# Kernel optimization log

Measured on AMD Instinct MI355X. Metric: run time of the kernel, lower is better.

Reference implementation:

```python
import jax, jax.numpy as jnp
import numpy as np

B, T, C = 4, 2048, 1024
E, F, K = 8, 2048, 2


def setup_inputs() -> dict:
    key = jax.random.key(0)
    k0, k1, k2, k3 = jax.random.split(key, 4)
    s = lambda d: 1.0 / np.sqrt(d)
    x = jax.random.normal(k0, (B, T, C), dtype=jnp.float32)
    Wr = jax.random.normal(k1, (E, C), dtype=jnp.float32) * s(C)      # router: nn.Linear(C, E) weight [E, C]
    W1 = jax.random.normal(k2, (E, 2 * F, C), dtype=jnp.float32) * s(C)  # per-expert w1 [2F, C]
    W2 = jax.random.normal(k3, (E, C, F), dtype=jnp.float32) * s(F)      # per-expert w2 [C, F]
    return {"x": x, "Wr": Wr, "W1": W1, "W2": W2}


def reference(x, Wr, W1, W2):
    Bb, Tt, Cc = x.shape
    flat = x.reshape(-1, Cc)                         # [N, C]
    N = flat.shape[0]
    # router: top-k then softmax over the k selected logits
    logits = flat @ Wr.T                             # [N, E]
    weights, ids = jax.lax.top_k(logits, K)          # [N, K]
    weights = jax.nn.softmax(weights, axis=-1)
    rows = jnp.arange(N)[:, None]
    router_weights = jnp.zeros((N, E), dtype=flat.dtype).at[rows, ids].add(weights)  # [N, E]
    # all experts on all tokens (dense reference), SwiGLU
    h = jnp.einsum('nc,efc->nef', flat, W1)          # [N, E, 2F]
    val, gate = h[..., :F], h[..., F:]
    act = val * jax.nn.silu(gate)                    # [N, E, F]
    expert_outputs = jnp.einsum('nef,ecf->nec', act, W2)  # [N, E, C]
    out = jnp.einsum('nec,ne->nc', expert_outputs, router_weights)
    return out.reshape(Bb, Tt, Cc)
```

## Files before the change

### kernel.cpp

```cpp
#include <hip/hip_runtime.h>

#define NTOK 8192
#define CDIM 1024
#define FDIM 2048
#define NEXP 8
#define CAP  16384
#define NPAIR 16384
#define MTCAP 32

typedef __bf16 bf16x8 __attribute__((ext_vector_type(8)));
typedef float  f32x4  __attribute__((ext_vector_type(4)));

__device__ __forceinline__ unsigned short f2bf(float f) {
    unsigned int u = __builtin_bit_cast(unsigned int, f);
    unsigned int r = (u + 0x7FFFu + ((u >> 16) & 1u)) >> 16;
    return (unsigned short)r;
}

__device__ __forceinline__ unsigned int pack2(float lo, float hi) {
    return ((unsigned int)f2bf(hi) << 16) | (unsigned int)f2bf(lo);
}

__device__ __forceinline__ float bflo(unsigned int u) {
    return __builtin_bit_cast(float, u << 16);
}
__device__ __forceinline__ float bfhi(unsigned int u) {
    return __builtin_bit_cast(float, u & 0xFFFF0000u);
}

__device__ __forceinline__ void gload_lds16(const void* g, void* l) {
    __builtin_amdgcn_global_load_lds(
        (const __attribute__((address_space(1))) unsigned int*)g,
        (__attribute__((address_space(3))) unsigned int*)l, 16, 0, 0);
}

#define BARRIER() asm volatile("s_barrier" ::: "memory")
#define WAIT_LGKM0() do { asm volatile("s_waitcnt lgkmcnt(0)" ::: "memory"); __builtin_amdgcn_sched_barrier(0); } while (0)
#define WAITVM0() asm volatile("s_waitcnt vmcnt(0)" ::: "memory")

__global__ void cvt_kernel(const float* __restrict__ s, unsigned short* __restrict__ d, long ngrp) {
    long i = (long)blockIdx.x * blockDim.x + threadIdx.x;
    long stride = (long)gridDim.x * blockDim.x;
    const float4* s4 = (const float4*)s;
    uint4* d4 = (uint4*)d;
    for (long g = i; g < ngrp; g += stride) {
        float4 a = s4[2 * g], b = s4[2 * g + 1];
        uint4 o;
        o.x = pack2(a.x, a.y); o.y = pack2(a.z, a.w);
        o.z = pack2(b.x, b.y); o.w = pack2(b.z, b.w);
        d4[g] = o;
    }
}

__global__ __launch_bounds__(256) void logits_kernel(
    const float* __restrict__ x, const float* __restrict__ Wr,
    float* __restrict__ wgt, int* __restrict__ eids)
{
    int w = threadIdx.x >> 6, l = threadIdx.x & 63;
    int t = blockIdx.x * 4 + w;
    const float* xr = x + (size_t)t * CDIM;
    float acc[NEXP];
    #pragma unroll
    for (int e = 0; e < NEXP; e++) acc[e] = 0.f;
    for (int c = l; c < CDIM; c += 64) {
        float xv = xr[c];
        #pragma unroll
        for (int e = 0; e < NEXP; e++) acc[e] += xv * Wr[e * CDIM + c];
    }
    #pragma unroll
    for (int e = 0; e < NEXP; e++)
        for (int off = 32; off > 0; off >>= 1) acc[e] += __shfl_down(acc[e], off);
    if (l == 0) {
        int i0 = 0; float l0 = acc[0];
        #pragma unroll
        for (int e = 1; e < NEXP; e++) if (acc[e] > l0) { l0 = acc[e]; i0 = e; }
        int i1 = -1; float l1 = -3.4e38f;
        #pragma unroll
        for (int e = 0; e < NEXP; e++) if (e != i0 && acc[e] > l1) { l1 = acc[e]; i1 = e; }
        float tv = __expf(l1 - l0);
        float den = 1.f + tv;
        wgt[2 * t] = 1.f / den;
        wgt[2 * t + 1] = tv / den;
        eids[t] = i0 | (i1 << 8);
    }
}

__global__ __launch_bounds__(256) void bucket_kernel(
    const int* __restrict__ eids, int* __restrict__ list, int* __restrict__ cnt)
{
    __shared__ int lcnt[NEXP];
    __shared__ int lbase[NEXP];
    int t = threadIdx.x;
    if (t < NEXP) lcnt[t] = 0;
    __syncthreads();
    int tok = blockIdx.x * 256 + t;
    int id = eids[tok];
    int e0 = id & 0xff, e1 = (id >> 8) & 0xff;
    int s0 = atomicAdd(&lcnt[e0], 1);
    int s1 = atomicAdd(&lcnt[e1], 1);
    __syncthreads();
    if (t < NEXP) lbase[t] = atomicAdd(&cnt[t], lcnt[t]);
    __syncthreads();
    list[e0 * CAP + lbase[e0] + s0] = 2 * tok;
    list[e1 * CAP + lbase[e1] + s1] = 2 * tok + 1;
}

__global__ void offs_kernel(const int* __restrict__ cnt, int* __restrict__ offs) {
    if (threadIdx.x == 0) {
        int a = 0;
        for (int e = 0; e < NEXP; e++) { offs[e] = a; a += cnt[e]; }
    }
}

__global__ __launch_bounds__(256) void pack_kernel(
    const float* __restrict__ x, const int* __restrict__ list,
    const int* __restrict__ cnt, const int* __restrict__ offs,
    const float* __restrict__ wgt,
    unsigned short* __restrict__ xg, float* __restrict__ wgs)
{
    int e = blockIdx.y;
    int cnt_e = cnt[e];
    int s0 = blockIdx.x * 16;
    if (s0 >= cnt_e) return;
    int t = threadIdx.x;
    int sr = s0 + (t >> 4);
    if (sr >= cnt_e) return;
    int p = list[e * CAP + sr];
    int tok = p >> 1;
    if ((t & 15) == 0) wgs[offs[e] + sr] = wgt[p];
    const float4* src = (const float4*)(x + (size_t)tok * CDIM);
    uint2* dst = (uint2*)(xg + (size_t)(offs[e] + sr) * CDIM);
    int c = t & 15;
    #pragma unroll
    for (int i = 0; i < 16; i++) {
        float4 v = src[c + i * 16];
        uint2 o; o.x = pack2(v.x, v.y); o.y = pack2(v.z, v.w);
        dst[c + i * 16] = o;
    }
}

__global__ __launch_bounds__(256, 2) void gemm1_kernel(
    const unsigned short* __restrict__ xg,
    const unsigned short* __restrict__ W1b,
    const float* __restrict__ wgs,
    unsigned short* __restrict__ act,
    const int* __restrict__ cnt, const int* __restrict__ offs)
{
    int e = blockIdx.z, nt = blockIdx.x, mt = blockIdx.y;
    int cnt_e = cnt[e];
    if (mt * 128 >= cnt_e) return;
    int off_e = offs[e];

    __shared__ __align__(16) char lds[32768];

    int t = threadIdx.x, l = t & 63, w = t >> 6;
    int wave_m = w >> 1, wave_n = w & 1;

    int c2s = ((t & 3) * 16) ^ (((t >> 5) & 1) << 5);
    int dst = t * 16;

    const char *sA0, *sA1, *sBv, *sBg;
    {
        int r0 = min(mt * 128 + (t >> 2), cnt_e - 1);
        int r1 = min(mt * 128 + 64 + (t >> 2), cnt_e - 1);
        sA0 = (const char*)xg + (size_t)(off_e + r0) * 2048 + c2s;
        sA1 = (const char*)xg + (size_t)(off_e + r1) * 2048 + c2s;
        int f = nt * 64 + (t >> 2);
        sBv = (const char*)W1b + ((size_t)e * 2 * FDIM + f) * 2048 + c2s;
        sBg = sBv + (size_t)FDIM * 2048;
    }

    int lane_off = (l & 15) * 64 + (((l >> 4) * 16) ^ (((l >> 3) & 1) << 5));
    f32x4 accV[4][2] = {}, accG[4][2] = {};

#define G1_STAGE(KB) do { \
        gload_lds16(sA0 + (KB),      (char*)lds + dst); \
        gload_lds16(sA1 + (KB),      (char*)lds + 4096 + dst); \
        gload_lds16(sA0 + (KB) + 64, (char*)lds + 8192 + dst); \
        gload_lds16(sA1 + (KB) + 64, (char*)lds + 12288 + dst); \
        gload_lds16(sBv + (KB),      (char*)lds + 16384 + dst); \
        gload_lds16(sBv + (KB) + 64, (char*)lds + 20480 + dst); \
        gload_lds16(sBg + (KB),      (char*)lds + 24576 + dst); \
        gload_lds16(sBg + (KB) + 64, (char*)lds + 28672 + dst); \
    } while (0)

    G1_STAGE(0);

    for (int kt = 0; kt < 16; kt++) {
        WAITVM0();
        BARRIER();

        bf16x8 af[2][4], bv[2][2], bg[2][2];
        #pragma unroll
        for (int h = 0; h < 2; h++) {
            #pragma unroll
            for (int m = 0; m < 4; m++)
                af[h][m] = *(const bf16x8*)((char*)lds + h * 8192 + (wave_m * 4 + m) * 1024 + lane_off);
            #pragma unroll
            for (int n = 0; n < 2; n++) {
                bv[h][n] = *(const bf16x8*)((char*)lds + 16384 + h * 4096 + (wave_n * 2 + n) * 1024 + lane_off);
                bg[h][n] = *(const bf16x8*)((char*)lds + 24576 + h * 4096 + (wave_n * 2 + n) * 1024 + lane_off);
            }
        }
        WAIT_LGKM0();
        BARRIER();

        if (kt != 15) { int kb = (kt + 1) * 128; G1_STAGE(kb); }
        __builtin_amdgcn_sched_barrier(0);

        __builtin_amdgcn_s_setprio(1);
        #pragma unroll
        for (int h = 0; h < 2; h++)
            #pragma unroll
            for (int m = 0; m < 4; m++)
                #pragma unroll
                for (int n = 0; n < 2; n++) {
                    accV[m][n] = __builtin_amdgcn_mfma_f32_16x16x32_bf16(af[h][m], bv[h][n], accV[m][n], 0, 0, 0);
                    accG[m][n] = __builtin_amdgcn_mfma_f32_16x16x32_bf16(af[h][m], bg[h][n], accG[m][n], 0, 0, 0);
                }
        __builtin_amdgcn_s_setprio(0);
    }
#undef G1_STAGE

    int colF = nt * 64 + wave_n * 32 + (l & 15);
    int rowB = mt * 128 + wave_m * 64 + ((l >> 4) * 4);
    #pragma unroll
    for (int m = 0; m < 4; m++) {
        #pragma unroll
        for (int r = 0; r < 4; r++) {
            int srow = rowB + m * 16 + r;
            if (srow < cnt_e) {
                float wsc = wgs[off_e + srow];
                #pragma unroll
                for (int n = 0; n < 2; n++) {
                    float g = accG[m][n][r];
                    float v = accV[m][n][r];
                    float aa = wsc * v * g / (1.f + __expf(-g));
                    act[(size_t)(off_e + srow) * FDIM + colF + n * 16] = f2bf(aa);
                }
            }
        }
    }
}

__global__ __launch_bounds__(256, 2) void gemm2_kernel(
    const unsigned short* __restrict__ act,
    const unsigned short* __restrict__ W2b,
    const int* __restrict__ list, const int* __restrict__ cnt,
    const int* __restrict__ offs,
    unsigned short* __restrict__ eob)
{
    int e = blockIdx.z, nt = blockIdx.x, mt = blockIdx.y;
    int cnt_e = cnt[e];
    if (mt * 128 >= cnt_e) return;
    int off_e = offs[e];
    const int* le = list + e * CAP;

    __shared__ __align__(16) char lds[32768];

    int t = threadIdx.x, l = t & 63, w = t >> 6;
    int wave_m = w >> 1, wave_n = w & 1;

    int c2s = ((t & 3) * 16) ^ (((t >> 5) & 1) << 5);
    int dst = t * 16;

    const char *sA0, *sA1, *sB0, *sB1;
    {
        int r0 = min(mt * 128 + (t >> 2), cnt_e - 1);
        int r1 = min(mt * 128 + 64 + (t >> 2), cnt_e - 1);
        sA0 = (const char*)act + (size_t)(off_e + r0) * 4096 + c2s;
        sA1 = (const char*)act + (size_t)(off_e + r1) * 4096 + c2s;
        int c0 = nt * 128 + (t >> 2);
        sB0 = (const char*)W2b + ((size_t)e * CDIM + c0) * 4096 + c2s;
        sB1 = sB0 + (size_t)64 * 4096;
    }

    int lane_off = (l & 15) * 64 + (((l >> 4) * 16) ^ (((l >> 3) & 1) << 5));
    f32x4 acc[4][4] = {};

#define G2_STAGE(KB) do { \
        gload_lds16(sA0 + (KB),      (char*)lds + dst); \
        gload_lds16(sA1 + (KB),      (char*)lds + 4096 + dst); \
        gload_lds16(sA0 + (KB) + 64, (char*)lds + 8192 + dst); \
        gload_lds16(sA1 + (KB) + 64, (char*)lds + 12288 + dst); \
        gload_lds16(sB0 + (KB),      (char*)lds + 16384 + dst); \
        gload_lds16(sB1 + (KB),      (char*)lds + 20480 + dst); \
        gload_lds16(sB0 + (KB) + 64, (char*)lds + 24576 + dst); \
        gload_lds16(sB1 + (KB) + 64, (char*)lds + 28672 + dst); \
    } while (0)

    G2_STAGE(0);

    for (int kt = 0; kt < 32; kt++) {
        WAITVM0();
        BARRIER();

        bf16x8 af[2][4], bf[2][4];
        #pragma unroll
        for (int h = 0; h < 2; h++) {
            #pragma unroll
            for (int m = 0; m < 4; m++)
                af[h][m] = *(const bf16x8*)((char*)lds + h * 8192 + (wave_m * 4 + m) * 1024 + lane_off);
            #pragma unroll
            for (int n = 0; n < 4; n++)
                bf[h][n] = *(const bf16x8*)((char*)lds + 16384 + h * 8192 + (wave_n * 4 + n) * 1024 + lane_off);
        }
        WAIT_LGKM0();
        BARRIER();

        if (kt != 31) { int kb = (kt + 1) * 128; G2_STAGE(kb); }
        __builtin_amdgcn_sched_barrier(0);

        __builtin_amdgcn_s_setprio(1);
        #pragma unroll
        for (int h = 0; h < 2; h++)
            #pragma unroll
            for (int m = 0; m < 4; m++)
                #pragma unroll
                for (int n = 0; n < 4; n++)
                    acc[m][n] = __builtin_amdgcn_mfma_f32_16x16x32_bf16(af[h][m], bf[h][n], acc[m][n], 0, 0, 0);
        __builtin_amdgcn_s_setprio(0);
    }
#undef G2_STAGE

    int colC = nt * 128 + wave_n * 64 + (l & 15);
    int rowB = mt * 128 + wave_m * 64 + ((l >> 4) * 4);
    #pragma unroll
    for (int m = 0; m < 4; m++) {
        #pragma unroll
        for (int r = 0; r < 4; r++) {
            int srow = rowB + m * 16 + r;
            if (srow < cnt_e) {
                int p = le[srow];
                #pragma unroll
                for (int n = 0; n < 4; n++)
                    eob[(size_t)p * CDIM + colC + n * 16] = f2bf(acc[m][n][r]);
            }
        }
    }
}

__global__ __launch_bounds__(256) void combine_kernel(
    const unsigned short* __restrict__ eob, float* __restrict__ out)
{
    const long NG = (long)NTOK * (CDIM / 4);
    long i = (long)blockIdx.x * blockDim.x + threadIdx.x;
    long stride = (long)gridDim.x * blockDim.x;
    float4* out4 = (float4*)out;
    for (long g = i; g < NG; g += stride) {
        long t = g >> 8;
        long j = g & 255;
        uint2 a = ((const uint2*)(eob + (size_t)(2 * t) * CDIM))[j];
        uint2 b = ((const uint2*)(eob + (size_t)(2 * t + 1) * CDIM))[j];
        float4 o;
        o.x = bflo(a.x) + bflo(b.x);
        o.y = bfhi(a.x) + bfhi(b.x);
        o.z = bflo(a.y) + bflo(b.y);
        o.w = bfhi(a.y) + bfhi(b.y);
        out4[g] = o;
    }
}

extern "C" void kernel_launch(void* const* d_in, const int* in_sizes, int n_in,
                              void* d_out, int out_size, void* d_ws, size_t ws_size,
                              hipStream_t stream) {
    const float* x  = (const float*)d_in[0];
    const float* Wr = (const float*)d_in[1];
    const float* W1 = (const float*)d_in[2];
    const float* W2 = (const float*)d_in[3];
    float* out = (float*)d_out;
    char* ws = (char*)d_ws;

    const size_t OFF_XG   = 0;
    const size_t OFF_W1B  = OFF_XG  + (size_t)NPAIR * CDIM * 2;
    const size_t OFF_ACT  = OFF_W1B + (size_t)NEXP * 2 * FDIM * CDIM * 2;
    const size_t OFF_LIST = OFF_ACT + (size_t)NPAIR * FDIM * 2;
    const size_t OFF_WGT  = OFF_LIST + (size_t)NEXP * CAP * 4;
    const size_t OFF_WGS  = OFF_WGT + (size_t)NPAIR * 4;
    const size_t OFF_CNT  = OFF_WGS + (size_t)NPAIR * 4;
    const size_t OFF_OFFS = OFF_CNT + 32;
    const size_t OFF_EIDS = OFF_OFFS + 32;

    unsigned short* xg  = (unsigned short*)(ws + OFF_XG);
    unsigned short* W1b = (unsigned short*)(ws + OFF_W1B);
    unsigned short* act = (unsigned short*)(ws + OFF_ACT);
    int*   list = (int*)(ws + OFF_LIST);
    float* wgt  = (float*)(ws + OFF_WGT);
    float* wgs  = (float*)(ws + OFF_WGS);
    int*   cnt  = (int*)(ws + OFF_CNT);
    int*   offs = (int*)(ws + OFF_OFFS);
    int*   eids = (int*)(ws + OFF_EIDS);
    unsigned short* W2b = (unsigned short*)(ws + OFF_W1B);
    unsigned short* eob = (unsigned short*)(ws + OFF_XG);

    hipMemsetAsync(cnt, 0, NEXP * sizeof(int), stream);

    cvt_kernel<<<4096, 256, 0, stream>>>(W1, W1b, (long)NEXP * 2 * FDIM * CDIM / 8);
    logits_kernel<<<NTOK / 4, 256, 0, stream>>>(x, Wr, wgt, eids);
    bucket_kernel<<<NTOK / 256, 256, 0, stream>>>(eids, list, cnt);
    offs_kernel<<<1, 64, 0, stream>>>(cnt, offs);
    pack_kernel<<<dim3(256, NEXP), 256, 0, stream>>>(x, list, cnt, offs, wgt, xg, wgs);

    gemm1_kernel<<<dim3(FDIM / 64, MTCAP, NEXP), 256, 0, stream>>>(xg, W1b, wgs, act, cnt, offs);

    cvt_kernel<<<4096, 256, 0, stream>>>(W2, W2b, (long)NEXP * CDIM * FDIM / 8);

    gemm2_kernel<<<dim3(CDIM / 128, MTCAP, NEXP), 256, 0, stream>>>(act, W2b, list, cnt, offs, eob);
    combine_kernel<<<2048, 256, 0, stream>>>(eob, out);
}
```

Before: 358.1 us.

## Double-buffer LDS stages in both expert GEMMs to prefetch two K-tiles ahead

Both grouped GEMM kernels now use two 32 KB LDS buffers and issue global-to-LDS loads two K-steps ahead, waiting with vmcnt(8) so one stage stays in flight while the current one is consumed. This hides more global memory latency behind the MFMA work instead of draining all loads every iteration. LDS per block doubles to 64 KB, which at two blocks per CU may reduce occupancy or conflict with the launch bound.

After: 367.9 us. 2.8% more time.

```diff
diff --git a/kernel.cpp b/kernel.cpp
--- a/kernel.cpp
+++ b/kernel.cpp
@@ -36,7 +36,7 @@
 
 #define BARRIER() asm volatile("s_barrier" ::: "memory")
 #define WAIT_LGKM0() do { asm volatile("s_waitcnt lgkmcnt(0)" ::: "memory"); __builtin_amdgcn_sched_barrier(0); } while (0)
-#define WAITVM0() asm volatile("s_waitcnt vmcnt(0)" ::: "memory")
+#define WAITVM(n) asm volatile("s_waitcnt vmcnt(" #n ")" ::: "memory")
 
 __global__ void cvt_kernel(const float* __restrict__ s, unsigned short* __restrict__ d, long ngrp) {
     long i = (long)blockIdx.x * blockDim.x + threadIdx.x;
@@ -151,7 +151,7 @@
     if (mt * 128 >= cnt_e) return;
     int off_e = offs[e];
 
-    __shared__ __align__(16) char lds[32768];
+    __shared__ __align__(16) char lds[65536];
 
     int t = threadIdx.x, l = t & 63, w = t >> 6;
     int wave_m = w >> 1, wave_n = w & 1;
@@ -173,39 +173,41 @@
     int lane_off = (l & 15) * 64 + (((l >> 4) * 16) ^ (((l >> 3) & 1) << 5));
     f32x4 accV[4][2] = {}, accG[4][2] = {};
 
-#define G1_STAGE(KB) do { \
-        gload_lds16(sA0 + (KB),      (char*)lds + dst); \
-        gload_lds16(sA1 + (KB),      (char*)lds + 4096 + dst); \
-        gload_lds16(sA0 + (KB) + 64, (char*)lds + 8192 + dst); \
-        gload_lds16(sA1 + (KB) + 64, (char*)lds + 12288 + dst); \
-        gload_lds16(sBv + (KB),      (char*)lds + 16384 + dst); \
-        gload_lds16(sBv + (KB) + 64, (char*)lds + 20480 + dst); \
-        gload_lds16(sBg + (KB),      (char*)lds + 24576 + dst); \
-        gload_lds16(sBg + (KB) + 64, (char*)lds + 28672 + dst); \
+#define G1_STAGE(BUF, KB) do { \
+        gload_lds16(sA0 + (KB),      (BUF) + dst); \
+        gload_lds16(sA1 + (KB),      (BUF) + 4096 + dst); \
+        gload_lds16(sA0 + (KB) + 64, (BUF) + 8192 + dst); \
+        gload_lds16(sA1 + (KB) + 64, (BUF) + 12288 + dst); \
+        gload_lds16(sBv + (KB),      (BUF) + 16384 + dst); \
+        gload_lds16(sBv + (KB) + 64, (BUF) + 20480 + dst); \
+        gload_lds16(sBg + (KB),      (BUF) + 24576 + dst); \
+        gload_lds16(sBg + (KB) + 64, (BUF) + 28672 + dst); \
     } while (0)
 
-    G1_STAGE(0);
+    G1_STAGE((char*)lds, 0);
+    G1_STAGE((char*)lds + 32768, 128);
 
     for (int kt = 0; kt < 16; kt++) {
-        WAITVM0();
+        if (kt == 15) { WAITVM(0); } else { WAITVM(8); }
         BARRIER();
 
+        char* Cur = (char*)lds + (kt & 1) * 32768;
         bf16x8 af[2][4], bv[2][2], bg[2][2];
         #pragma unroll
         for (int h = 0; h < 2; h++) {
             #pragma unroll
             for (int m = 0; m < 4; m++)
-                af[h][m] = *(const bf16x8*)((char*)lds + h * 8192 + (wave_m * 4 + m) * 1024 + lane_off);
+                af[h][m] = *(const bf16x8*)(Cur + h * 8192 + (wave_m * 4 + m) * 1024 + lane_off);
             #pragma unroll
             for (int n = 0; n < 2; n++) {
-                bv[h][n] = *(const bf16x8*)((char*)lds + 16384 + h * 4096 + (wave_n * 2 + n) * 1024 + lane_off);
-                bg[h][n] = *(const bf16x8*)((char*)lds + 24576 + h * 4096 + (wave_n * 2 + n) * 1024 + lane_off);
+                bv[h][n] = *(const bf16x8*)(Cur + 16384 + h * 4096 + (wave_n * 2 + n) * 1024 + lane_off);
+                bg[h][n] = *(const bf16x8*)(Cur + 24576 + h * 4096 + (wave_n * 2 + n) * 1024 + lane_off);
             }
         }
         WAIT_LGKM0();
         BARRIER();
 
-        if (kt != 15) { int kb = (kt + 1) * 128; G1_STAGE(kb); }
+        if (kt < 14) G1_STAGE(Cur, (kt + 2) * 128);
         __builtin_amdgcn_sched_barrier(0);
 
         __builtin_amdgcn_s_setprio(1);
@@ -256,7 +258,7 @@
     int off_e = offs[e];
     const int* le = list + e * CAP;
 
-    __shared__ __align__(16) char lds[32768];
+    __shared__ __align__(16) char lds[65536];
 
     int t = threadIdx.x, l = t & 63, w = t >> 6;
     int wave_m = w >> 1, wave_n = w & 1;
@@ -278,37 +280,39 @@
     int lane_off = (l & 15) * 64 + (((l >> 4) * 16) ^ (((l >> 3) & 1) << 5));
     f32x4 acc[4][4] = {};
 
-#define G2_STAGE(KB) do { \
-        gload_lds16(sA0 + (KB),      (char*)lds + dst); \
-        gload_lds16(sA1 + (KB),      (char*)lds + 4096 + dst); \
-        gload_lds16(sA0 + (KB) + 64, (char*)lds + 8192 + dst); \
-        gload_lds16(sA1 + (KB) + 64, (char*)lds + 12288 + dst); \
-        gload_lds16(sB0 + (KB),      (char*)lds + 16384 + dst); \
-        gload_lds16(sB1 + (KB),      (char*)lds + 20480 + dst); \
-        gload_lds16(sB0 + (KB) + 64, (char*)lds + 24576 + dst); \
-        gload_lds16(sB1 + (KB) + 64, (char*)lds + 28672 + dst); \
+#define G2_STAGE(BUF, KB) do { \
+        gload_lds16(sA0 + (KB),      (BUF) + dst); \
+        gload_lds16(sA1 + (KB),      (BUF) + 4096 + dst); \
+        gload_lds16(sA0 + (KB) + 64, (BUF) + 8192 + dst); \
+        gload_lds16(sA1 + (KB) + 64, (BUF) + 12288 + dst); \
+        gload_lds16(sB0 + (KB),      (BUF) + 16384 + dst); \
+        gload_lds16(sB1 + (KB),      (BUF) + 20480 + dst); \
+        gload_lds16(sB0 + (KB) + 64, (BUF) + 24576 + dst); \
+        gload_lds16(sB1 + (KB) + 64, (BUF) + 28672 + dst); \
     } while (0)
 
-    G2_STAGE(0);
+    G2_STAGE((char*)lds, 0);
+    G2_STAGE((char*)lds + 32768, 128);
 
     for (int kt = 0; kt < 32; kt++) {
-        WAITVM0();
+        if (kt == 31) { WAITVM(0); } else { WAITVM(8); }
         BARRIER();
 
+        char* Cur = (char*)lds + (kt & 1) * 32768;
         bf16x8 af[2][4], bf[2][4];
         #pragma unroll
         for (int h = 0; h < 2; h++) {
             #pragma unroll
             for (int m = 0; m < 4; m++)
-                af[h][m] = *(const bf16x8*)((char*)lds + h * 8192 + (wave_m * 4 + m) * 1024 + lane_off);
+                af[h][m] = *(const bf16x8*)(Cur + h * 8192 + (wave_m * 4 + m) * 1024 + lane_off);
             #pragma unroll
             for (int n = 0; n < 4; n++)
-                bf[h][n] = *(const bf16x8*)((char*)lds + 16384 + h * 8192 + (wave_n * 4 + n) * 1024 + lane_off);
+                bf[h][n] = *(const bf16x8*)(Cur + 16384 + h * 8192 + (wave_n * 4 + n) * 1024 + lane_off);
         }
         WAIT_LGKM0();
         BARRIER();
 
-        if (kt != 31) { int kb = (kt + 1) * 128; G2_STAGE(kb); }
+        if (kt < 30) G2_STAGE(Cur, (kt + 2) * 128);
         __builtin_amdgcn_sched_barrier(0);
 
         __builtin_amdgcn_s_setprio(1);
```

## Double-buffer LDS in expert GEMMs with two-stage prefetch and partial vmcnt waits

Applied to the files above, without the earlier changes.

Both expert GEMM kernels now split each 128-wide K chunk into two 64-wide halves. Each half goes into one of two LDS buffers, and the next-but-one half is prefetched while the current one is computed. The loads are no longer fully drained each iteration: the loop waits with vmcnt(4), so one stage of global-to-LDS loads stays in flight during the MFMAs. The cost is twice as many loop iterations and barriers, each doing half the MFMA work per sync. The loops are also fully unrolled, which increases code size.

After: 380.6 us. +6.3%, slower.

```diff
diff --git a/kernel.cpp b/kernel.cpp
--- a/kernel.cpp
+++ b/kernel.cpp
@@ -36,7 +36,7 @@
 
 #define BARRIER() asm volatile("s_barrier" ::: "memory")
 #define WAIT_LGKM0() do { asm volatile("s_waitcnt lgkmcnt(0)" ::: "memory"); __builtin_amdgcn_sched_barrier(0); } while (0)
-#define WAITVM0() asm volatile("s_waitcnt vmcnt(0)" ::: "memory")
+#define WAITVM(n) asm volatile("s_waitcnt vmcnt(" #n ")" ::: "memory")
 
 __global__ void cvt_kernel(const float* __restrict__ s, unsigned short* __restrict__ d, long ngrp) {
     long i = (long)blockIdx.x * blockDim.x + threadIdx.x;
@@ -173,51 +173,46 @@
     int lane_off = (l & 15) * 64 + (((l >> 4) * 16) ^ (((l >> 3) & 1) << 5));
     f32x4 accV[4][2] = {}, accG[4][2] = {};
 
-#define G1_STAGE(KB) do { \
-        gload_lds16(sA0 + (KB),      (char*)lds + dst); \
-        gload_lds16(sA1 + (KB),      (char*)lds + 4096 + dst); \
-        gload_lds16(sA0 + (KB) + 64, (char*)lds + 8192 + dst); \
-        gload_lds16(sA1 + (KB) + 64, (char*)lds + 12288 + dst); \
-        gload_lds16(sBv + (KB),      (char*)lds + 16384 + dst); \
-        gload_lds16(sBv + (KB) + 64, (char*)lds + 20480 + dst); \
-        gload_lds16(sBg + (KB),      (char*)lds + 24576 + dst); \
-        gload_lds16(sBg + (KB) + 64, (char*)lds + 28672 + dst); \
+#define G1_STAGE(H) do { \
+        char* Hb = (char*)lds + ((H) & 1) * 16384; \
+        gload_lds16(sA0 + (H) * 64, Hb + dst); \
+        gload_lds16(sA1 + (H) * 64, Hb + 4096 + dst); \
+        gload_lds16(sBv + (H) * 64, Hb + 8192 + dst); \
+        gload_lds16(sBg + (H) * 64, Hb + 12288 + dst); \
     } while (0)
 
     G1_STAGE(0);
-
-    for (int kt = 0; kt < 16; kt++) {
-        WAITVM0();
+    G1_STAGE(1);
+
+    #pragma unroll
+    for (int kt = 0; kt < 32; kt++) {
+        if (kt == 31) { WAITVM(0); } else { WAITVM(4); }
         BARRIER();
 
-        bf16x8 af[2][4], bv[2][2], bg[2][2];
-        #pragma unroll
-        for (int h = 0; h < 2; h++) {
-            #pragma unroll
-            for (int m = 0; m < 4; m++)
-                af[h][m] = *(const bf16x8*)((char*)lds + h * 8192 + (wave_m * 4 + m) * 1024 + lane_off);
-            #pragma unroll
-            for (int n = 0; n < 2; n++) {
-                bv[h][n] = *(const bf16x8*)((char*)lds + 16384 + h * 4096 + (wave_n * 2 + n) * 1024 + lane_off);
-                bg[h][n] = *(const bf16x8*)((char*)lds + 24576 + h * 4096 + (wave_n * 2 + n) * 1024 + lane_off);
-            }
+        const char* H = (const char*)lds + (kt & 1) * 16384;
+        bf16x8 af[4], bv[2], bg[2];
+        #pragma unroll
+        for (int m = 0; m < 4; m++)
+            af[m] = *(const bf16x8*)(H + (wave_m * 4 + m) * 1024 + lane_off);
+        #pragma unroll
+        for (int n = 0; n < 2; n++) {
+            bv[n] = *(const bf16x8*)(H + 8192 + (wave_n * 2 + n) * 1024 + lane_off);
+            bg[n] = *(const bf16x8*)(H + 12288 + (wave_n * 2 + n) * 1024 + lane_off);
         }
         WAIT_LGKM0();
         BARRIER();
 
-        if (kt != 15) { int kb = (kt + 1) * 128; G1_STAGE(kb); }
+        if (kt < 30) G1_STAGE(kt + 2);
         __builtin_amdgcn_sched_barrier(0);
 
         __builtin_amdgcn_s_setprio(1);
         #pragma unroll
-        for (int h = 0; h < 2; h++)
+        for (int m = 0; m < 4; m++)
             #pragma unroll
-            for (int m = 0; m < 4; m++)
-                #pragma unroll
-                for (int n = 0; n < 2; n++) {
-                    accV[m][n] = __builtin_amdgcn_mfma_f32_16x16x32_bf16(af[h][m], bv[h][n], accV[m][n], 0, 0, 0);
-                    accG[m][n] = __builtin_amdgcn_mfma_f32_16x16x32_bf16(af[h][m], bg[h][n], accG[m][n], 0, 0, 0);
-                }
+            for (int n = 0; n < 2; n++) {
+                accV[m][n] = __builtin_amdgcn_mfma_f32_16x16x32_bf16(af[m], bv[n], accV[m][n], 0, 0, 0);
+                accG[m][n] = __builtin_amdgcn_mfma_f32_16x16x32_bf16(af[m], bg[n], accG[m][n], 0, 0, 0);
+            }
         __builtin_amdgcn_s_setprio(0);
     }
 #undef G1_STAGE
@@ -278,47 +273,42 @@
     int lane_off = (l & 15) * 64 + (((l >> 4) * 16) ^ (((l >> 3) & 1) << 5));
     f32x4 acc[4][4] = {};
 
-#define G2_STAGE(KB) do { \
-        gload_lds16(sA0 + (KB),      (char*)lds + dst); \
-        gload_lds16(sA1 + (KB),      (char*)lds + 4096 + dst); \
-        gload_lds16(sA0 + (KB) + 64, (char*)lds + 8192 + dst); \
-        gload_lds16(sA1 + (KB) + 64, (char*)lds + 12288 + dst); \
-        gload_lds16(sB0 + (KB),      (char*)lds + 16384 + dst); \
-        gload_lds16(sB1 + (KB),      (char*)lds + 20480 + dst); \
-        gload_lds16(sB0 + (KB) + 64, (char*)lds + 24576 + dst); \
-        gload_lds16(sB1 + (KB) + 64, (char*)lds + 28672 + dst); \
+#define G2_STAGE(H) do { \
+        char* Hb = (char*)lds + ((H) & 1) * 16384; \
+        gload_lds16(sA0 + (H) * 64, Hb + dst); \
+        gload_lds16(sA1 + (H) * 64, Hb + 4096 + dst); \
+        gload_lds16(sB0 + (H) * 64, Hb + 8192 + dst); \
+        gload_lds16(sB1 + (H) * 64, Hb + 12288 + dst); \
     } while (0)
 
     G2_STAGE(0);
-
-    for (int kt = 0; kt < 32; kt++) {
-        WAITVM0();
+    G2_STAGE(1);
+
+    #pragma unroll
+    for (int kt = 0; kt < 64; kt++) {
+        if (kt == 63) { WAITVM(0); } else { WAITVM(4); }
         BARRIER();
 
-        bf16x8 af[2][4], bf[2][4];
-        #pragma unroll
-        for (int h = 0; h < 2; h++) {
-            #pragma unroll
-            for (int m = 0; m < 4; m++)
-                af[h][m] = *(const bf16x8*)((char*)lds + h * 8192 + (wave_m * 4 + m) * 1024 + lane_off);
+        const char* H = (const char*)lds + (kt & 1) * 16384;
+        bf16x8 af[4], bf[4];
+        #pragma unroll
+        for (int m = 0; m < 4; m++)
+            af[m] = *(const bf16x8*)(H + (wave_m * 4 + m) * 1024 + lane_off);
+        #pragma unroll
+        for (int n = 0; n < 4; n++)
+            bf[n] = *(const bf16x8*)(H + 8192 + (wave_n * 4 + n) * 1024 + lane_off);
+        WAIT_LGKM0();
+        BARRIER();
+
+        if (kt < 62) G2_STAGE(kt + 2);
+        __builtin_amdgcn_sched_barrier(0);
+
+        __builtin_amdgcn_s_setprio(1);
+        #pragma unroll
+        for (int m = 0; m < 4; m++)
             #pragma unroll
             for (int n = 0; n < 4; n++)
-                bf[h][n] = *(const bf16x8*)((char*)lds + 16384 + h * 8192 + (wave_n * 4 + n) * 1024 + lane_off);
-        }
-        WAIT_LGKM0();
-        BARRIER();
-
-        if (kt != 31) { int kb = (kt + 1) * 128; G2_STAGE(kb); }
-        __builtin_amdgcn_sched_barrier(0);
-
-        __builtin_amdgcn_s_setprio(1);
-        #pragma unroll
-        for (int h = 0; h < 2; h++)
-            #pragma unroll
-            for (int m = 0; m < 4; m++)
-                #pragma unroll
-                for (int n = 0; n < 4; n++)
-                    acc[m][n] = __builtin_amdgcn_mfma_f32_16x16x32_bf16(af[h][m], bf[h][n], acc[m][n], 0, 0, 0);
+                acc[m][n] = __builtin_amdgcn_mfma_f32_16x16x32_bf16(af[m], bf[n], acc[m][n], 0, 0, 0);
         __builtin_amdgcn_s_setprio(0);
     }
 #undef G2_STAGE
```
